# Kernel tuning notes

Measured on AMD Instinct MI355X. Metric: run time of the kernel, lower is better.

Reference implementation:

```python
import jax, jax.numpy as jnp
import numpy as np

B, N, E, D, H = 32, 2048, 1024, 1024, 1024


def setup_inputs() -> dict:
    key = jax.random.key(0)
    k_enc, k_dec, k_we, k_wd, k_wo = jax.random.split(key, 5)
    enc = jax.random.normal(k_enc, (B, N, E), dtype=jnp.float32)
    dec = jax.random.normal(k_dec, (B, D), dtype=jnp.float32)
    inp_mask = jnp.ones((B, N), dtype=bool)
    # params initialized like torch.rand -> uniform [0,1)
    w_e = jax.random.uniform(k_we, (E, H), dtype=jnp.float32)
    w_d = jax.random.uniform(k_wd, (D, H), dtype=jnp.float32)
    w_out = jax.random.uniform(k_wo, (H, 1), dtype=jnp.float32)
    return {"enc": enc, "dec": dec, "inp_mask": inp_mask,
            "w_e": w_e, "w_d": w_d, "w_out": w_out}


def reference(enc, dec, inp_mask, w_e, w_d, w_out):
    # hidden: [B, N, H]
    h = jnp.tanh(enc @ w_e + (dec @ w_d)[:, None, :])
    scores = (h @ w_out)[..., 0]                      # [B, N]
    scores = jnp.where(inp_mask, scores, -jnp.inf)    # mask invalid positions
    probs = jax.nn.softmax(scores, axis=-1)           # [B, N]
    attn = jnp.einsum('bn,bne->be', probs, enc)       # weighted sum of enc
    return attn, probs
```

## Files before the change

### kernel.cpp

```cpp
#include <hip/hip_runtime.h>
#include <hip/hip_bf16.h>

typedef _Float16 half8 __attribute__((ext_vector_type(8)));
typedef float f32x4 __attribute__((ext_vector_type(4)));

#define Bsz 32
#define Nseq 2048
#define Edim 1024
#define Hdim 1024

__device__ __forceinline__ void gload_lds16(const void* g, void* l) {
    __builtin_amdgcn_global_load_lds(
        (const __attribute__((address_space(1))) unsigned int*)g,
        (__attribute__((address_space(3))) unsigned int*)l, 16, 0, 0);
}

__global__ void k_dw(const float* __restrict__ dec, const float* __restrict__ w_d,
                     float* __restrict__ dw) {
    int b = blockIdx.x;
    int h = blockIdx.y * 256 + threadIdx.x;
    const float* dr = dec + b * 1024;
    float a0 = 0.f, a1 = 0.f, a2 = 0.f, a3 = 0.f;
    for (int d = 0; d < 1024; d += 4) {
        a0 += dr[d + 0] * w_d[(d + 0) * 1024 + h];
        a1 += dr[d + 1] * w_d[(d + 1) * 1024 + h];
        a2 += dr[d + 2] * w_d[(d + 2) * 1024 + h];
        a3 += dr[d + 3] * w_d[(d + 3) * 1024 + h];
    }
    dw[b * 1024 + h] = (a0 + a1) + (a2 + a3);
}

__global__ void k_split(const float* __restrict__ w_e,
                        _Float16* __restrict__ w_hiT, _Float16* __restrict__ w_loT) {
    __shared__ _Float16 th[32][33];
    __shared__ _Float16 tl[32][33];
    int e0 = blockIdx.x * 32, h0 = blockIdx.y * 32;
    int tx = threadIdx.x & 31, ty = threadIdx.x >> 5;
#pragma unroll
    for (int i = 0; i < 4; ++i) {
        int r = ty + i * 8;
        float x = w_e[(size_t)(e0 + r) * 1024 + h0 + tx];
        _Float16 h = (_Float16)x;
        th[r][tx] = h;
        tl[r][tx] = (_Float16)(x - (float)h);
    }
    __syncthreads();
#pragma unroll
    for (int i = 0; i < 4; ++i) {
        int r = ty + i * 8;
        w_hiT[(size_t)(h0 + r) * 1024 + e0 + tx] = th[tx][r];
        w_loT[(size_t)(h0 + r) * 1024 + e0 + tx] = tl[tx][r];
    }
}

__global__ __launch_bounds__(512, 2)
void k_scores(const float* __restrict__ enc,
              const _Float16* __restrict__ w_hiT, const _Float16* __restrict__ w_loT,
              const float* __restrict__ dw, const float* __restrict__ w_out,
              float* __restrict__ scores) {
    extern __shared__ __align__(16) char smem[];
    float* scoreL = (float*)(smem + 131072);

    const int tid  = threadIdx.x;
    const int lane = tid & 63;
    const int wave = tid >> 6;
    const int wr = wave >> 2, wc = wave & 3;
    const int m0 = blockIdx.x * 256;
    const int bb = m0 >> 11;
    const float* dwb = dw + bb * 1024;

    const int a_row = tid >> 2, a_ks = tid & 3;
    const float* aBase = enc + (size_t)(m0 + a_row) * 1024 + a_ks * 8;
    const int b_row = tid & 255, b_ks = tid >> 8;
    const _Float16* bhBase = w_hiT + (size_t)b_row * 1024 + b_ks * 8;
    const _Float16* blBase = w_loT + (size_t)b_row * 1024 + b_ks * 8;
    const int wofs = wave * 1024;

    if (tid < 256) scoreL[tid] = 0.f;

    f32x4 acc[8][4];
#pragma unroll
    for (int m = 0; m < 8; ++m)
#pragma unroll
        for (int n = 0; n < 4; ++n) acc[m][n] = (f32x4){0.f, 0.f, 0.f, 0.f};

    float4 pa0, pa1, pa2, pa3;

#define A_LOAD(t) do { \
        const float* _p = aBase + (((t) & 31) << 5); \
        pa0 = ((const float4*)_p)[0]; \
        pa1 = ((const float4*)_p)[1]; \
        const float* _p2 = _p + 128 * 1024; \
        pa2 = ((const float4*)_p2)[0]; \
        pa3 = ((const float4*)_p2)[1]; \
    } while (0)
#define B_ISSUE(t, buf) do { \
        const size_t _g = ((size_t)((t) >> 5) << 18) + (size_t)(((t) & 31) << 5); \
        char* _b = smem + 65536 + (buf) * 32768; \
        gload_lds16(bhBase + _g,      _b + wofs); \
        gload_lds16(bhBase + _g + 16, _b + 8192 + wofs); \
        gload_lds16(blBase + _g,      _b + 16384 + wofs); \
        gload_lds16(blBase + _g + 16, _b + 24576 + wofs); \
    } while (0)
#define A_STAGE(buf) do { \
        float _q[16] = {pa0.x, pa0.y, pa0.z, pa0.w, pa1.x, pa1.y, pa1.z, pa1.w, \
                        pa2.x, pa2.y, pa2.z, pa2.w, pa3.x, pa3.y, pa3.z, pa3.w}; \
        half8 _hi0, _lo0, _hi1, _lo1; \
        _Pragma("unroll") \
        for (int _j = 0; _j < 8; ++_j) { \
            _Float16 _h = (_Float16)_q[_j]; \
            _hi0[_j] = _h; \
            _lo0[_j] = (_Float16)(_q[_j] - (float)_h); \
            _Float16 _h2 = (_Float16)_q[_j + 8]; \
            _hi1[_j] = _h2; \
            _lo1[_j] = (_Float16)(_q[_j + 8] - (float)_h2); \
        } \
        char* _a = smem + (buf) * 32768; \
        *(half8*)(_a + a_ks * 4096 + a_row * 16) = _hi0; \
        *(half8*)(_a + 16384 + a_ks * 4096 + a_row * 16) = _lo0; \
        *(half8*)(_a + a_ks * 4096 + (a_row + 128) * 16) = _hi1; \
        *(half8*)(_a + 16384 + a_ks * 4096 + (a_row + 128) * 16) = _lo1; \
    } while (0)

    A_LOAD(0);
    B_ISSUE(0, 0);
    A_STAGE(0);
    A_LOAD(1);
    __syncthreads();

    const int ks = lane >> 4, rb = lane & 15;

    for (int t = 0; t < 128; ++t) {
        const int cur = t & 1;
        if (t < 127) {
            B_ISSUE(t + 1, cur ^ 1);
            A_STAGE(cur ^ 1);
            if (t < 126) A_LOAD(t + 2);
        }
        const char* sa = smem + cur * 32768;
        const char* sb = smem + 65536 + cur * 32768;
        half8 bh[4], bl[4];
#pragma unroll
        for (int n = 0; n < 4; ++n) {
            int off = ks * 4096 + (wc * 64 + n * 16 + rb) * 16;
            bh[n] = *(const half8*)(sb + off);
            bl[n] = *(const half8*)(sb + 16384 + off);
        }
        __builtin_amdgcn_s_setprio(1);
#pragma unroll
        for (int m = 0; m < 8; ++m) {
            int off = ks * 4096 + (wr * 128 + m * 16 + rb) * 16;
            half8 ah = *(const half8*)(sa + off);
            half8 al = *(const half8*)(sa + 16384 + off);
#pragma unroll
            for (int n = 0; n < 4; ++n) {
                acc[m][n] = __builtin_amdgcn_mfma_f32_16x16x32_f16(ah, bh[n], acc[m][n], 0, 0, 0);
                acc[m][n] = __builtin_amdgcn_mfma_f32_16x16x32_f16(ah, bl[n], acc[m][n], 0, 0, 0);
                acc[m][n] = __builtin_amdgcn_mfma_f32_16x16x32_f16(al, bh[n], acc[m][n], 0, 0, 0);
            }
        }
        __builtin_amdgcn_s_setprio(0);

        if ((t & 31) == 31) {
            const int h0 = (t >> 5) << 8;
#pragma unroll
            for (int m = 0; m < 8; ++m) {
                float con[4] = {0.f, 0.f, 0.f, 0.f};
#pragma unroll
                for (int n = 0; n < 4; ++n) {
                    int h = h0 + wc * 64 + n * 16 + rb;
                    float dwv = dwb[h];
                    float wo  = w_out[h];
#pragma unroll
                    for (int r = 0; r < 4; ++r) {
                        float x = acc[m][n][r] + dwv;
                        float e = __expf(2.0f * fabsf(x));
                        float th = copysignf(1.0f - __fdividef(2.0f, e + 1.0f), x);
                        con[r] += th * wo;
                    }
                    acc[m][n] = (f32x4){0.f, 0.f, 0.f, 0.f};
                }
#pragma unroll
                for (int r = 0; r < 4; ++r) {
                    float v = con[r];
                    v += __shfl_xor(v, 1);
                    v += __shfl_xor(v, 2);
                    v += __shfl_xor(v, 4);
                    v += __shfl_xor(v, 8);
                    con[r] = v;
                }
                if ((lane & 15) == 0) {
                    int rbase = wr * 128 + m * 16 + (lane >> 4) * 4;
#pragma unroll
                    for (int r = 0; r < 4; ++r)
                        atomicAdd(&scoreL[rbase + r], con[r]);
                }
            }
        }
        __syncthreads();
    }

    __syncthreads();
    if (tid < 256) scores[m0 + tid] = scoreL[tid];
#undef A_LOAD
#undef B_ISSUE
#undef A_STAGE
}

__global__ void k_softmax(const float* __restrict__ scores,
                          const int* __restrict__ mask,
                          float* __restrict__ probs, float* __restrict__ out_probs) {
    int b = blockIdx.x, tid = threadIdx.x;
    __shared__ float red[8];
    float v[8];
    float m = -INFINITY;
#pragma unroll
    for (int i = 0; i < 8; ++i) {
        int n = tid + i * 256;
        float s = scores[b * 2048 + n];
        s = (mask[b * 2048 + n] != 0) ? s : -INFINITY;
        v[i] = s;
        m = fmaxf(m, s);
    }
    for (int off = 32; off; off >>= 1) m = fmaxf(m, __shfl_xor(m, off));
    if ((tid & 63) == 0) red[tid >> 6] = m;
    __syncthreads();
    m = fmaxf(fmaxf(red[0], red[1]), fmaxf(red[2], red[3]));
    float sum = 0.f;
#pragma unroll
    for (int i = 0; i < 8; ++i) {
        v[i] = expf(v[i] - m);
        sum += v[i];
    }
    for (int off = 32; off; off >>= 1) sum += __shfl_xor(sum, off);
    if ((tid & 63) == 0) red[4 + (tid >> 6)] = sum;
    __syncthreads();
    sum = red[4] + red[5] + red[6] + red[7];
    float inv = 1.0f / sum;
#pragma unroll
    for (int i = 0; i < 8; ++i) {
        int n = tid + i * 256;
        float p = v[i] * inv;
        probs[b * 2048 + n]     = p;
        out_probs[b * 2048 + n] = p;
    }
}

__global__ void k_attn(const float* __restrict__ probs, const float* __restrict__ enc,
                       float* __restrict__ attn) {
    __shared__ float pv[128];
    __shared__ int   pidx[128];
    __shared__ int   cnt;
    int b = blockIdx.x, c = blockIdx.y, t = threadIdx.x;
    if (t == 0) cnt = 0;
    __syncthreads();
    if (t < 128) {
        float p = probs[b * 2048 + c * 128 + t];
        if (p >= 1e-12f) {
            int slot = atomicAdd(&cnt, 1);
            pv[slot]   = p;
            pidx[slot] = c * 128 + t;
        }
    }
    __syncthreads();
    int nk = cnt;
    if (nk == 0) return;
    const float* eb = enc + (size_t)b * 2048 * 1024;
    float4 acc = {0.f, 0.f, 0.f, 0.f};
    for (int i = 0; i < nk; ++i) {
        float p = pv[i];
        float4 v = ((const float4*)(eb + (size_t)pidx[i] * 1024))[t];
        acc.x += p * v.x;
        acc.y += p * v.y;
        acc.z += p * v.z;
        acc.w += p * v.w;
    }
    float* o = attn + b * 1024 + t * 4;
    atomicAdd(o + 0, acc.x);
    atomicAdd(o + 1, acc.y);
    atomicAdd(o + 2, acc.z);
    atomicAdd(o + 3, acc.w);
}

extern "C" void kernel_launch(void* const* d_in, const int* in_sizes, int n_in,
                              void* d_out, int out_size, void* d_ws, size_t ws_size,
                              hipStream_t stream) {
    const float* enc   = (const float*)d_in[0];
    const float* dec   = (const float*)d_in[1];
    const int*   mask  = (const int*)d_in[2];
    const float* w_e   = (const float*)d_in[3];
    const float* w_d   = (const float*)d_in[4];
    const float* w_out = (const float*)d_in[5];

    float* out_attn  = (float*)d_out;
    float* out_probs = out_attn + Bsz * Hdim;

    float* dw        = (float*)d_ws;
    float* scores    = dw + Bsz * Hdim;
    float* probs     = scores + Bsz * Nseq;
    _Float16* w_hiT  = (_Float16*)(probs + Bsz * Nseq);
    _Float16* w_loT  = w_hiT + Edim * Hdim;

    static const int kScoresLds = 132096;
    hipFuncSetAttribute((const void*)k_scores,
                        hipFuncAttributeMaxDynamicSharedMemorySize, kScoresLds);

    hipMemsetAsync(out_attn, 0, Bsz * Hdim * sizeof(float), stream);
    k_dw<<<dim3(32, 4), dim3(256), 0, stream>>>(dec, w_d, dw);
    k_split<<<dim3(32, 32), dim3(256), 0, stream>>>(w_e, w_hiT, w_loT);
    k_scores<<<dim3(256), dim3(512), kScoresLds, stream>>>(enc, w_hiT, w_loT, dw, w_out, scores);
    k_softmax<<<dim3(32), dim3(256), 0, stream>>>(scores, mask, probs, out_probs);
    k_attn<<<dim3(32, 16), dim3(256), 0, stream>>>(probs, enc, out_attn);
}
```

Baseline: 496.3 us.

## Interleave global-to-LDS prefetch with MFMA phases using explicit waitcnt and barriers

Splits the main GEMM k-step into four phases, each loading two A fragments and doing paired MFMAs. The next tile's B-hi, B-lo, A staging and A global loads are spread across those phases. __syncthreads is replaced by raw s_barrier with hand-placed s_waitcnt counts, so memory traffic overlaps compute instead of being issued up front. This relies on correct manual vmcnt/lgkmcnt accounting, and the extra barriers per iteration add synchronization cost.

```diff
diff --git a/kernel.cpp b/kernel.cpp
--- a/kernel.cpp
+++ b/kernel.cpp
@@ -94,11 +94,15 @@
         pa2 = ((const float4*)_p2)[0]; \
         pa3 = ((const float4*)_p2)[1]; \
     } while (0)
-#define B_ISSUE(t, buf) do { \
+#define B_ISSUE_HI(t, buf) do { \
         const size_t _g = ((size_t)((t) >> 5) << 18) + (size_t)(((t) & 31) << 5); \
         char* _b = smem + 65536 + (buf) * 32768; \
         gload_lds16(bhBase + _g,      _b + wofs); \
         gload_lds16(bhBase + _g + 16, _b + 8192 + wofs); \
+    } while (0)
+#define B_ISSUE_LO(t, buf) do { \
+        const size_t _g = ((size_t)((t) >> 5) << 18) + (size_t)(((t) & 31) << 5); \
+        char* _b = smem + 65536 + (buf) * 32768; \
         gload_lds16(blBase + _g,      _b + 16384 + wofs); \
         gload_lds16(blBase + _g + 16, _b + 24576 + wofs); \
     } while (0)
@@ -121,44 +125,93 @@
         *(half8*)(_a + a_ks * 4096 + (a_row + 128) * 16) = _hi1; \
         *(half8*)(_a + 16384 + a_ks * 4096 + (a_row + 128) * 16) = _lo1; \
     } while (0)
+#define LOAD_A_FRAG(rh, rl, m) do { \
+        int _off = ks * 4096 + (wr * 128 + (m) * 16 + rb) * 16; \
+        rh = *(const half8*)(sa + _off); \
+        rl = *(const half8*)(sa + 16384 + _off); \
+    } while (0)
+#define MFMA_PAIR(mb) do { \
+        _Pragma("unroll") \
+        for (int n = 0; n < 4; ++n) { \
+            acc[(mb)][n]   = __builtin_amdgcn_mfma_f32_16x16x32_f16(ah0, bh[n], acc[(mb)][n], 0, 0, 0); \
+            acc[(mb)][n]   = __builtin_amdgcn_mfma_f32_16x16x32_f16(ah0, bl[n], acc[(mb)][n], 0, 0, 0); \
+            acc[(mb)][n]   = __builtin_amdgcn_mfma_f32_16x16x32_f16(al0, bh[n], acc[(mb)][n], 0, 0, 0); \
+            acc[(mb)+1][n] = __builtin_amdgcn_mfma_f32_16x16x32_f16(ah1, bh[n], acc[(mb)+1][n], 0, 0, 0); \
+            acc[(mb)+1][n] = __builtin_amdgcn_mfma_f32_16x16x32_f16(ah1, bl[n], acc[(mb)+1][n], 0, 0, 0); \
+            acc[(mb)+1][n] = __builtin_amdgcn_mfma_f32_16x16x32_f16(al1, bh[n], acc[(mb)+1][n], 0, 0, 0); \
+        } \
+    } while (0)
+#define WAITLG0 do { asm volatile("s_waitcnt lgkmcnt(0)" ::: "memory"); \
+                     __builtin_amdgcn_sched_barrier(0); } while (0)
 
     A_LOAD(0);
-    B_ISSUE(0, 0);
+    B_ISSUE_HI(0, 0);
+    B_ISSUE_LO(0, 0);
     A_STAGE(0);
     A_LOAD(1);
-    __syncthreads();
+    asm volatile("s_waitcnt vmcnt(0) lgkmcnt(0)" ::: "memory");
+    __builtin_amdgcn_sched_barrier(0);
+    __builtin_amdgcn_s_barrier();
 
     const int ks = lane >> 4, rb = lane & 15;
 
     for (int t = 0; t < 128; ++t) {
         const int cur = t & 1;
-        if (t < 127) {
-            B_ISSUE(t + 1, cur ^ 1);
-            A_STAGE(cur ^ 1);
-            if (t < 126) A_LOAD(t + 2);
-        }
         const char* sa = smem + cur * 32768;
         const char* sb = smem + 65536 + cur * 32768;
         half8 bh[4], bl[4];
+        half8 ah0, al0, ah1, al1;
+
+        LOAD_A_FRAG(ah0, al0, 0);
+        LOAD_A_FRAG(ah1, al1, 1);
 #pragma unroll
         for (int n = 0; n < 4; ++n) {
             int off = ks * 4096 + (wc * 64 + n * 16 + rb) * 16;
             bh[n] = *(const half8*)(sb + off);
             bl[n] = *(const half8*)(sb + 16384 + off);
         }
+        if (t < 127) B_ISSUE_HI(t + 1, cur ^ 1);
+        asm volatile("s_waitcnt lgkmcnt(8)" ::: "memory");
+        __builtin_amdgcn_sched_barrier(0);
+        __builtin_amdgcn_s_barrier();
+        WAITLG0;
         __builtin_amdgcn_s_setprio(1);
-#pragma unroll
-        for (int m = 0; m < 8; ++m) {
-            int off = ks * 4096 + (wr * 128 + m * 16 + rb) * 16;
-            half8 ah = *(const half8*)(sa + off);
-            half8 al = *(const half8*)(sa + 16384 + off);
-#pragma unroll
-            for (int n = 0; n < 4; ++n) {
-                acc[m][n] = __builtin_amdgcn_mfma_f32_16x16x32_f16(ah, bh[n], acc[m][n], 0, 0, 0);
-                acc[m][n] = __builtin_amdgcn_mfma_f32_16x16x32_f16(ah, bl[n], acc[m][n], 0, 0, 0);
-                acc[m][n] = __builtin_amdgcn_mfma_f32_16x16x32_f16(al, bh[n], acc[m][n], 0, 0, 0);
-            }
+        MFMA_PAIR(0);
+        __builtin_amdgcn_s_setprio(0);
+        __builtin_amdgcn_s_barrier();
+
+        LOAD_A_FRAG(ah0, al0, 2);
+        LOAD_A_FRAG(ah1, al1, 3);
+        if (t < 127) B_ISSUE_LO(t + 1, cur ^ 1);
+        __builtin_amdgcn_s_barrier();
+        WAITLG0;
+        __builtin_amdgcn_s_setprio(1);
+        MFMA_PAIR(2);
+        __builtin_amdgcn_s_setprio(0);
+        __builtin_amdgcn_s_barrier();
+
+        LOAD_A_FRAG(ah0, al0, 4);
+        LOAD_A_FRAG(ah1, al1, 5);
+        if (t < 127) A_STAGE(cur ^ 1);
+        __builtin_amdgcn_s_barrier();
+        WAITLG0;
+        __builtin_amdgcn_s_setprio(1);
+        MFMA_PAIR(4);
+        __builtin_amdgcn_s_setprio(0);
+        __builtin_amdgcn_s_barrier();
+
+        LOAD_A_FRAG(ah0, al0, 6);
+        LOAD_A_FRAG(ah1, al1, 7);
+        if (t < 126) A_LOAD(t + 2);
+        __builtin_amdgcn_s_barrier();
+        if (t < 126) {
+            asm volatile("s_waitcnt vmcnt(4) lgkmcnt(0)" ::: "memory");
+        } else {
+            asm volatile("s_waitcnt vmcnt(0) lgkmcnt(0)" ::: "memory");
         }
+        __builtin_amdgcn_sched_barrier(0);
+        __builtin_amdgcn_s_setprio(1);
+        MFMA_PAIR(6);
         __builtin_amdgcn_s_setprio(0);
 
         if ((t & 31) == 31) {
@@ -197,14 +250,18 @@
                 }
             }
         }
-        __syncthreads();
+        __builtin_amdgcn_s_barrier();
     }
 
     __syncthreads();
     if (tid < 256) scores[m0 + tid] = scoreL[tid];
 #undef A_LOAD
-#undef B_ISSUE
+#undef B_ISSUE_HI
+#undef B_ISSUE_LO
 #undef A_STAGE
+#undef LOAD_A_FRAG
+#undef MFMA_PAIR
+#undef WAITLG0
 }
 
 __global__ void k_softmax(const float* __restrict__ scores,
```

Measured after the change: 496.5 us. Within noise of the previous version (+0.0%).

## Stream fp32 enc tiles directly into LDS and split hi/lo after LDS read

Applied to the files above, without the earlier changes.

The A operand (enc) is no longer loaded into registers, split into fp16 hi/lo and written to LDS. Instead it is copied as raw fp32 into LDS with asynchronous global_load_lds, and each wave does the hi/lo split right after reading its fragment from LDS. A and B LDS layouts get XOR swizzles to avoid bank conflicts, and the setprio hints around the MFMA loop are removed. This takes register staging and the VALU conversion off the load path and lets A loads overlap like B loads. The cost is that the conversion is repeated by every wave sharing the same rows, and each fragment needs two LDS reads.

```diff
diff --git a/kernel.cpp b/kernel.cpp
--- a/kernel.cpp
+++ b/kernel.cpp
@@ -68,13 +68,14 @@
     const int m0 = blockIdx.x * 256;
     const int bb = m0 >> 11;
     const float* dwb = dw + bb * 1024;
-
-    const int a_row = tid >> 2, a_ks = tid & 3;
-    const float* aBase = enc + (size_t)(m0 + a_row) * 1024 + a_ks * 8;
-    const int b_row = tid & 255, b_ks = tid >> 8;
-    const _Float16* bhBase = w_hiT + (size_t)b_row * 1024 + b_ks * 8;
-    const _Float16* blBase = w_loT + (size_t)b_row * 1024 + b_ks * 8;
-    const int wofs = wave * 1024;
+    const int rb = lane & 15, ksl = lane >> 4;
+
+    const char* encB = (const char*)enc + (size_t)m0 * 4096;
+    const char* whiB = (const char*)w_hiT;
+    const char* wloB = (const char*)w_loT;
+
+    const int aAddr = ksl * 8192 + ((rb ^ ksl) << 5) + wr * 4096;
+    const int bAddr = ksl * 4096 + ((rb ^ (2 * ksl)) << 4) + wc * 1024;
 
     if (tid < 256) scoreL[tid] = 0.f;
 
@@ -84,74 +85,64 @@
 #pragma unroll
         for (int n = 0; n < 4; ++n) acc[m][n] = (f32x4){0.f, 0.f, 0.f, 0.f};
 
-    float4 pa0, pa1, pa2, pa3;
-
-#define A_LOAD(t) do { \
-        const float* _p = aBase + (((t) & 31) << 5); \
-        pa0 = ((const float4*)_p)[0]; \
-        pa1 = ((const float4*)_p)[1]; \
-        const float* _p2 = _p + 128 * 1024; \
-        pa2 = ((const float4*)_p2)[0]; \
-        pa3 = ((const float4*)_p2)[1]; \
+#define A_ISSUE(t, buf) do { \
+        const int _kt = (t) & 31; \
+        char* _d = smem + (buf) * 32768; \
+        _Pragma("unroll") \
+        for (int _k = 0; _k < 4; ++_k) { \
+            const char* _s = encB + (size_t)((tid >> 1) ^ _k) * 4096 \
+                           + (size_t)_kt * 128 + _k * 32 + (tid & 1) * 16; \
+            gload_lds16(_s, _d + _k * 8192 + tid * 16); \
+        } \
     } while (0)
 #define B_ISSUE(t, buf) do { \
-        const size_t _g = ((size_t)((t) >> 5) << 18) + (size_t)(((t) & 31) << 5); \
-        char* _b = smem + 65536 + (buf) * 32768; \
-        gload_lds16(bhBase + _g,      _b + wofs); \
-        gload_lds16(bhBase + _g + 16, _b + 8192 + wofs); \
-        gload_lds16(blBase + _g,      _b + 16384 + wofs); \
-        gload_lds16(blBase + _g + 16, _b + 24576 + wofs); \
+        const int _kt = (t) & 31; \
+        const size_t _h0 = (size_t)((t) >> 5) << 19; \
+        char* _d = smem + 65536 + (buf) * 32768; \
+        _Pragma("unroll") \
+        for (int _j = 0; _j < 2; ++_j) { \
+            const int _ks = 2 * _j + (tid >> 8); \
+            const size_t _ro = _h0 + (size_t)((tid & 255) ^ (2 * _ks)) * 2048 \
+                             + (size_t)_kt * 64 + _ks * 16; \
+            gload_lds16(whiB + _ro, _d + _j * 8192 + tid * 16); \
+            gload_lds16(wloB + _ro, _d + 16384 + _j * 8192 + tid * 16); \
+        } \
     } while (0)
-#define A_STAGE(buf) do { \
-        float _q[16] = {pa0.x, pa0.y, pa0.z, pa0.w, pa1.x, pa1.y, pa1.z, pa1.w, \
-                        pa2.x, pa2.y, pa2.z, pa2.w, pa3.x, pa3.y, pa3.z, pa3.w}; \
-        half8 _hi0, _lo0, _hi1, _lo1; \
-        _Pragma("unroll") \
-        for (int _j = 0; _j < 8; ++_j) { \
-            _Float16 _h = (_Float16)_q[_j]; \
-            _hi0[_j] = _h; \
-            _lo0[_j] = (_Float16)(_q[_j] - (float)_h); \
-            _Float16 _h2 = (_Float16)_q[_j + 8]; \
-            _hi1[_j] = _h2; \
-            _lo1[_j] = (_Float16)(_q[_j + 8] - (float)_h2); \
-        } \
-        char* _a = smem + (buf) * 32768; \
-        *(half8*)(_a + a_ks * 4096 + a_row * 16) = _hi0; \
-        *(half8*)(_a + 16384 + a_ks * 4096 + a_row * 16) = _lo0; \
-        *(half8*)(_a + a_ks * 4096 + (a_row + 128) * 16) = _hi1; \
-        *(half8*)(_a + 16384 + a_ks * 4096 + (a_row + 128) * 16) = _lo1; \
-    } while (0)
-
-    A_LOAD(0);
+
+    A_ISSUE(0, 0);
     B_ISSUE(0, 0);
-    A_STAGE(0);
-    A_LOAD(1);
-    __syncthreads();
-
-    const int ks = lane >> 4, rb = lane & 15;
+    __syncthreads();
 
     for (int t = 0; t < 128; ++t) {
         const int cur = t & 1;
         if (t < 127) {
+            A_ISSUE(t + 1, cur ^ 1);
             B_ISSUE(t + 1, cur ^ 1);
-            A_STAGE(cur ^ 1);
-            if (t < 126) A_LOAD(t + 2);
         }
         const char* sa = smem + cur * 32768;
         const char* sb = smem + 65536 + cur * 32768;
+
         half8 bh[4], bl[4];
 #pragma unroll
         for (int n = 0; n < 4; ++n) {
-            int off = ks * 4096 + (wc * 64 + n * 16 + rb) * 16;
-            bh[n] = *(const half8*)(sb + off);
-            bl[n] = *(const half8*)(sb + 16384 + off);
-        }
-        __builtin_amdgcn_s_setprio(1);
+            bh[n] = *(const half8*)(sb + bAddr + n * 256);
+            bl[n] = *(const half8*)(sb + 16384 + bAddr + n * 256);
+        }
 #pragma unroll
         for (int m = 0; m < 8; ++m) {
-            int off = ks * 4096 + (wr * 128 + m * 16 + rb) * 16;
-            half8 ah = *(const half8*)(sa + off);
-            half8 al = *(const half8*)(sa + 16384 + off);
+            f32x4 q0 = *(const f32x4*)(sa + aAddr + m * 512);
+            f32x4 q1 = *(const f32x4*)(sa + aAddr + m * 512 + 16);
+            half8 ah, al;
+#pragma unroll
+            for (int j = 0; j < 4; ++j) {
+                float v0 = q0[j], v1 = q1[j];
+                _Float16 h0 = (_Float16)v0;
+                ah[j] = h0;
+                al[j] = (_Float16)(v0 - (float)h0);
+                _Float16 h1 = (_Float16)v1;
+                ah[j + 4] = h1;
+                al[j + 4] = (_Float16)(v1 - (float)h1);
+            }
 #pragma unroll
             for (int n = 0; n < 4; ++n) {
                 acc[m][n] = __builtin_amdgcn_mfma_f32_16x16x32_f16(ah, bh[n], acc[m][n], 0, 0, 0);
@@ -159,7 +150,6 @@
                 acc[m][n] = __builtin_amdgcn_mfma_f32_16x16x32_f16(al, bh[n], acc[m][n], 0, 0, 0);
             }
         }
-        __builtin_amdgcn_s_setprio(0);
 
         if ((t & 31) == 31) {
             const int h0 = (t >> 5) << 8;
@@ -189,8 +179,8 @@
                     v += __shfl_xor(v, 8);
                     con[r] = v;
                 }
-                if ((lane & 15) == 0) {
-                    int rbase = wr * 128 + m * 16 + (lane >> 4) * 4;
+                if (rb == 0) {
+                    int rbase = wr * 128 + m * 16 + ksl * 4;
 #pragma unroll
                     for (int r = 0; r < 4; ++r)
                         atomicAdd(&scoreL[rbase + r], con[r]);
@@ -202,9 +192,8 @@
 
     __syncthreads();
     if (tid < 256) scores[m0 + tid] = scoreL[tid];
-#undef A_LOAD
+#undef A_ISSUE
 #undef B_ISSUE
-#undef A_STAGE
 }
 
 __global__ void k_softmax(const float* __restrict__ scores,
```

After: 528.5 us. 1.06x slower.
